# Performance work log

Measured on AMD Instinct MI355X. Metric: run time of the kernel, lower is better.

Reference implementation:

```python
import jax, jax.numpy as jnp
import numpy as np

B, T, H = 64, 512, 32
D_CONTENT, D_DISTORT, D_MOTION = 4096, 512, 256
D_TOTAL = D_CONTENT + D_DISTORT + D_MOTION  # 4864
RED = 128
TIME_INTERVAL = 8  # conf.ADJACENT_INTERVAL assumed
TAUS = (8, 10, 12, 14, 16)
BETA = 0.5


def setup_inputs() -> dict:
    key = jax.random.key(0)
    ks = jax.random.split(key, 20)
    s = 0.02
    f32 = jnp.float32
    return {
        "motionFeat": jax.random.normal(ks[0], (B, T, D_MOTION), f32),
        "featContent": jax.random.normal(ks[1], (B, T, D_CONTENT), f32),
        "featDistort": jax.random.normal(ks[2], (B, T, D_DISTORT), f32),
        "inputLength": jax.random.randint(ks[3], (B,), 200, T + 1),
        "fc0_w": jax.random.normal(ks[4], (RED, D_TOTAL), f32) * s,
        "fc0_b": jnp.zeros((RED,), f32),
        "gru_wih_f": jax.random.normal(ks[5], (3 * H, RED), f32) * s,
        "gru_whh_f": jax.random.normal(ks[6], (3 * H, H), f32) * s,
        "gru_bih_f": jnp.zeros((3 * H,), f32),
        "gru_bhh_f": jnp.zeros((3 * H,), f32),
        "gru_wih_b": jax.random.normal(ks[7], (3 * H, RED), f32) * s,
        "gru_whh_b": jax.random.normal(ks[8], (3 * H, H), f32) * s,
        "gru_bih_b": jnp.zeros((3 * H,), f32),
        "gru_bhh_b": jnp.zeros((3 * H,), f32),
        "q_w": jax.random.normal(ks[9], (1, 2 * H), f32) * s,
        "q_b": jnp.zeros((1,), f32),
        "mem1_w": jax.random.normal(ks[10], (32, 2 * H), f32) * s,
        "mem1_b": jnp.zeros((32,), f32),
        "mem2_w": jax.random.normal(ks[11], (5, 32), f32) * s,
        "mem2_b": jnp.zeros((5,), f32),
    }


def _gru_dir(xg, Whh, bhh, mask):
    """xg: [B,T,3H] precomputed input gates; mask: [B,T] bool. Returns [B,T,H]."""
    def step(h, inp):
        xgt, mt = inp  # [B,3H], [B]
        hg = h @ Whh.T + bhh
        r = jax.nn.sigmoid(xgt[:, :H] + hg[:, :H])
        z = jax.nn.sigmoid(xgt[:, H:2 * H] + hg[:, H:2 * H])
        n = jnp.tanh(xgt[:, 2 * H:] + r * hg[:, 2 * H:])
        hn = (1.0 - z) * n + z * h
        h = jnp.where(mt[:, None], hn, h)
        return h, h
    h0 = jnp.zeros((xg.shape[0], H), xg.dtype)
    _, out = jax.lax.scan(step, h0, (jnp.swapaxes(xg, 0, 1), jnp.swapaxes(mask, 0, 1)))
    return jnp.swapaxes(out, 0, 1)


def _tp_score(qv, maskf, vlen, tau, beta=BETA):
    """Vectorized TP() + mean over valid frames. qv,maskf: [B,T]; vlen: [B]."""
    Bq, Tq = qv.shape
    # l: causal running min over last tau frames (front pad +inf in q-space)
    qpad = jnp.concatenate([jnp.full((Bq, tau - 1), jnp.inf, qv.dtype), qv], axis=1)
    l = jnp.min(jnp.stack([qpad[:, k:k + Tq] for k in range(tau)], 0), axis=0)
    # m/n: forward exp-weighted average over next tau frames; padding qp=1e4 -> exp(-1e4)=0
    w = jnp.exp(-qv) * maskf
    num = qv * w
    zpad = jnp.zeros((Bq, tau - 1), qv.dtype)
    npad = jnp.concatenate([num, zpad], axis=1)
    wpad = jnp.concatenate([w, zpad], axis=1)
    msum = sum(npad[:, k:k + Tq] for k in range(tau))
    nsum = sum(wpad[:, k:k + Tq] for k in range(tau))
    ratio = jnp.where(nsum > 0, msum / jnp.where(nsum > 0, nsum, 1.0), 0.0)
    pooled = beta * ratio + (1.0 - beta) * l
    return jnp.sum(pooled * maskf, axis=1) / vlen.astype(qv.dtype)


def reference(motionFeat, featContent, featDistort, inputLength,
              fc0_w, fc0_b, gru_wih_f, gru_whh_f, gru_bih_f, gru_bhh_f,
              gru_wih_b, gru_whh_b, gru_bih_b, gru_bhh_b,
              q_w, q_b, mem1_w, mem1_b, mem2_w, mem2_b):
    total = jnp.concatenate([featContent, featDistort, motionFeat], axis=-1)  # [B,T,4864]
    scores = total @ fc0_w.T + fc0_b  # ANN with n_ANNlayers=1 -> just fc0
    vlen = inputLength - 2 * (TIME_INTERVAL // 2) - 1  # [B]
    t = jnp.arange(T)
    mask = t[None, :] < vlen[:, None]  # [B,T] bool
    maskf = mask.astype(scores.dtype)
    # forward GRU
    xg_f = scores @ gru_wih_f.T + gru_bih_f
    out_f = _gru_dir(xg_f, gru_whh_f, gru_bhh_f, mask)
    # backward GRU: reverse each sequence within its valid length
    rev = jnp.where(mask, vlen[:, None] - 1 - t[None, :], t[None, :])  # [B,T]
    x_rev = jnp.take_along_axis(scores, rev[:, :, None], axis=1)
    xg_b = x_rev @ gru_wih_b.T + gru_bih_b
    out_b_rev = _gru_dir(xg_b, gru_whh_b, gru_bhh_b, mask)
    out_b = jnp.take_along_axis(out_b_rev, rev[:, :, None], axis=1)
    outputs = jnp.concatenate([out_f, out_b], axis=-1) * maskf[:, :, None]  # [B,T,64]
    lastHidForward = jnp.take_along_axis(out_f, (vlen - 1)[:, None, None], axis=1)[:, 0]  # [B,32]
    lastHidBackward = out_b[:, 0]  # [B,32]
    q = (outputs @ q_w.T + q_b)[..., 0]  # [B,T]
    hidcat = jnp.concatenate([lastHidForward, lastHidBackward], axis=-1)
    h1 = jax.nn.relu(hidcat @ mem1_w.T + mem1_b)
    param = jax.nn.softmax(h1 @ mem2_w.T + mem2_b, axis=-1)  # [B,5]
    scores5 = jnp.stack([_tp_score(q, maskf, vlen, tau) for tau in TAUS], axis=-1)  # [B,5]
    one_hot = jax.nn.one_hot(jnp.argmax(param, axis=1), 5, dtype=scores5.dtype)
    finalScores = jnp.sum(one_hot * scores5, axis=-1)  # [B]
    return finalScores
```

## Files before the change

### kernel.cpp

```cpp
#include <hip/hip_runtime.h>

typedef float  floatx4  __attribute__((ext_vector_type(4)));
typedef float  floatx2  __attribute__((ext_vector_type(2)));
typedef __bf16 bf16x8   __attribute__((ext_vector_type(8)));
typedef unsigned short ushort8v __attribute__((ext_vector_type(8)));

constexpr int NB = 64;
constexpr int NT = 512;
constexpr int DC = 4096, DD = 512, DM = 256, DTOT = 4864;
constexpr int RED = 128;
constexpr int MROWS = NB * NT;

__device__ __forceinline__ unsigned short f2bf(float f) {
  unsigned u = __float_as_uint(f);
  unsigned r = u + 0x7FFFu + ((u >> 16) & 1u);
  return (unsigned short)(r >> 16);
}

__device__ __forceinline__ ushort8v pack8(floatx4 a, floatx4 b) {
  ushort8v u;
  u[0] = f2bf(a[0]); u[1] = f2bf(a[1]); u[2] = f2bf(a[2]); u[3] = f2bf(a[3]);
  u[4] = f2bf(b[0]); u[5] = f2bf(b[1]); u[6] = f2bf(b[2]); u[7] = f2bf(b[3]);
  return u;
}

template<int MODE>
__global__ __launch_bounds__(256, 2) void gemm_bt(
    const float* __restrict__ A0, const float* __restrict__ A1, const float* __restrict__ A2,
    const float* __restrict__ W0, const float* __restrict__ W1,
    const float* __restrict__ bias0, const float* __restrict__ bias1,
    float* __restrict__ outp)
{
  constexpr int BN   = (MODE == 0) ? 128 : 192;
  constexpr int KTOT = (MODE == 0) ? DTOT : RED;
  constexpr int WNT  = (MODE == 0) ? 2 : 3;
  constexpr int BK   = 128;
  constexpr int ACH  = 64 * (BK / 8) / 256;
  constexpr int WCH  = BN * (BK / 8) / 256;

  __shared__ __align__(16) unsigned short As[64 * BK];
  __shared__ __align__(16) unsigned short Ws[BN * BK];

  const int tid  = threadIdx.x;
  const int lane = tid & 63;
  const int wave = tid >> 6;
  const int m0   = blockIdx.x * 64;

  floatx4 pa[2 * ACH], pw[2 * WCH];

  auto loadA = [&](int k0) {
    #pragma unroll
    for (int c = 0; c < ACH; ++c) {
      const int g   = c * 256 + tid;
      const int row = g >> 4;
      const int kk  = (g & 15) * 8;
      const int m   = m0 + row;
      const float* src;
      if (MODE == 0) {
        const int k = k0 + kk;
        if (k < DC)           src = A0 + (size_t)m * DC + k;
        else if (k < DC + DD) src = A1 + (size_t)m * DD + (k - DC);
        else                  src = A2 + (size_t)m * DM + (k - DC - DD);
      } else {
        src = A0 + (size_t)m * RED + (k0 + kk);
      }
      pa[2 * c]     = *(const floatx4*)(src);
      pa[2 * c + 1] = *(const floatx4*)(src + 4);
    }
  };
  auto loadW = [&](int k0) {
    #pragma unroll
    for (int c = 0; c < WCH; ++c) {
      const int g   = c * 256 + tid;
      const int row = g >> 4;
      const int kk  = (g & 15) * 8;
      const float* src;
      if (MODE == 0) {
        src = W0 + (size_t)row * DTOT + (k0 + kk);
      } else {
        src = (row < 96) ? (W0 + (size_t)row * RED + (k0 + kk))
                         : (W1 + (size_t)(row - 96) * RED + (k0 + kk));
      }
      pw[2 * c]     = *(const floatx4*)(src);
      pw[2 * c + 1] = *(const floatx4*)(src + 4);
    }
  };
  auto storeA = [&]() {
    #pragma unroll
    for (int c = 0; c < ACH; ++c) {
      const int g   = c * 256 + tid;
      const int row = g >> 4;
      const int kk  = (g & 15) * 8;
      *(ushort8v*)&As[row * BK + (kk ^ ((row & 15) * 8))] = pack8(pa[2 * c], pa[2 * c + 1]);
    }
  };
  auto storeW = [&]() {
    #pragma unroll
    for (int c = 0; c < WCH; ++c) {
      const int g   = c * 256 + tid;
      const int row = g >> 4;
      const int kk  = (g & 15) * 8;
      *(ushort8v*)&Ws[row * BK + (kk ^ ((row & 15) * 8))] = pack8(pw[2 * c], pw[2 * c + 1]);
    }
  };

  floatx4 acc[4][WNT];
  #pragma unroll
  for (int mt = 0; mt < 4; ++mt)
    #pragma unroll
    for (int nt = 0; nt < WNT; ++nt)
      acc[mt][nt] = (floatx4){0.f, 0.f, 0.f, 0.f};

  const int lrow = lane & 15;
  const int lko  = (lane >> 4) * 8;

  loadA(0); loadW(0);

  for (int k0 = 0; k0 < KTOT; k0 += BK) {
    storeA(); storeW();
    __syncthreads();
    if (k0 + BK < KTOT) { loadA(k0 + BK); loadW(k0 + BK); }
    #pragma unroll
    for (int kk = 0; kk < BK; kk += 32) {
      bf16x8 af[4];
      #pragma unroll
      for (int mt = 0; mt < 4; ++mt) {
        const int row = mt * 16 + lrow;
        af[mt] = __builtin_bit_cast(bf16x8,
            *(const ushort8v*)&As[row * BK + ((kk + lko) ^ ((row & 15) * 8))]);
      }
      #pragma unroll
      for (int nt = 0; nt < WNT; ++nt) {
        const int wrow = (wave * WNT + nt) * 16 + lrow;
        bf16x8 wf = __builtin_bit_cast(bf16x8,
            *(const ushort8v*)&Ws[wrow * BK + ((kk + lko) ^ ((wrow & 15) * 8))]);
        #pragma unroll
        for (int mt = 0; mt < 4; ++mt)
          acc[mt][nt] = __builtin_amdgcn_mfma_f32_16x16x32_bf16(af[mt], wf, acc[mt][nt], 0, 0, 0);
      }
    }
    __syncthreads();
  }

  #pragma unroll
  for (int nt = 0; nt < WNT; ++nt) {
    const int n = (wave * WNT + nt) * 16 + lrow;
    const float bv = (MODE == 0) ? bias0[n]
                                 : ((n < 96) ? bias0[n] : bias1[n - 96]);
    #pragma unroll
    for (int mt = 0; mt < 4; ++mt) {
      const int mr = m0 + mt * 16 + (lane >> 4) * 4;
      #pragma unroll
      for (int r = 0; r < 4; ++r)
        outp[(size_t)(mr + r) * BN + n] = acc[mt][nt][r] + bv;
    }
  }
}

__global__ __launch_bounds__(64) void gru_kernel(
    const float* __restrict__ xg,
    const float* __restrict__ whh_f, const float* __restrict__ whh_b,
    const float* __restrict__ bhh_f, const float* __restrict__ bhh_b,
    const float* __restrict__ q_w,
    const int* __restrict__ inputLength,
    float* __restrict__ qpart,
    float* __restrict__ hid)
{
  const int b    = blockIdx.x >> 1;
  const int dir  = blockIdx.x & 1;
  const int l    = threadIdx.x;
  const int half = l >> 5;
  const int row  = l & 31;
  const int vlen = inputLength[b] - 9;

  const float* whh = dir ? whh_b : whh_f;
  const float* bhh = dir ? bhh_b : bhh_f;

  __shared__ __align__(16) float hsh[32];

  floatx2 wr[8], wz[8], wn[8];
  #pragma unroll
  for (int j = 0; j < 8; ++j) {
    const int c = 16 * half + 2 * j;
    wr[j] = *(const floatx2*)&whh[(size_t)row        * 32 + c];
    wz[j] = *(const floatx2*)&whh[(size_t)(32 + row) * 32 + c];
    wn[j] = *(const floatx2*)&whh[(size_t)(64 + row) * 32 + c];
  }
  const float br = bhh[row], bz = bhh[32 + row], bn = bhh[64 + row];
  const float qw = q_w[dir * 32 + row];

  if (l < 32) hsh[l] = 0.f;
  __syncthreads();

  auto xaddr = [&](int tt) {
    const int time = dir ? (vlen - 1 - tt) : tt;
    return xg + (size_t)(b * NT + time) * 192 + dir * 96;
  };
  float c_r = 0.f, c_z = 0.f, c_n = 0.f, n_r = 0.f, n_z = 0.f, n_n = 0.f;
  if (l < 32) {
    const float* x0 = xaddr(0);
    c_r = x0[l]; c_z = x0[32 + l]; c_n = x0[64 + l];
    if (vlen > 1) {
      const float* x1 = xaddr(1);
      n_r = x1[l]; n_z = x1[32 + l]; n_n = x1[64 + l];
    }
  }

  float* qout = qpart + (size_t)dir * (NB * NT) + (size_t)b * NT;

  float hl = 0.f;
  for (int t = 0; t < vlen; ++t) {
    const int time = dir ? (vlen - 1 - t) : t;

    float f_r = 0.f, f_z = 0.f, f_n = 0.f;
    if (t + 2 < vlen && l < 32) {
      const float* x2 = xaddr(t + 2);
      f_r = x2[l]; f_z = x2[32 + l]; f_n = x2[64 + l];
    }

    float h[16];
    #pragma unroll
    for (int i = 0; i < 4; ++i)
      *(floatx4*)&h[4 * i] = *(const floatx4*)&hsh[16 * half + 4 * i];
    const floatx2* h2 = (const floatx2*)h;

    floatx2 ar = {0.f, 0.f}, az = {0.f, 0.f}, an = {0.f, 0.f};
    floatx2 ar1 = {0.f, 0.f}, az1 = {0.f, 0.f}, an1 = {0.f, 0.f};
    #pragma unroll
    for (int j = 0; j < 4; ++j) {
      ar  += wr[j]     * h2[j];     ar1 += wr[4 + j] * h2[4 + j];
      az  += wz[j]     * h2[j];     az1 += wz[4 + j] * h2[4 + j];
      an  += wn[j]     * h2[j];     an1 += wn[4 + j] * h2[4 + j];
    }
    float pr = ar[0] + ar[1] + ar1[0] + ar1[1];
    float pz = az[0] + az[1] + az1[0] + az1[1];
    float pn = an[0] + an[1] + an1[0] + an1[1];
    pr += __shfl_xor(pr, 32);
    pz += __shfl_xor(pz, 32);
    pn += __shfl_xor(pn, 32);

    float hn = hl;
    if (l < 32) {
      const float r = 1.f / (1.f + __expf(-(c_r + pr + br)));
      const float z = 1.f / (1.f + __expf(-(c_z + pz + bz)));
      const float e = __expf(-2.f * (c_n + r * (pn + bn)));
      const float n = 2.f / (1.f + e) - 1.f;
      hn = (1.f - z) * n + z * hl;
      hl = hn;
      hsh[l] = hn;
    }

    float qp = (l < 32) ? hn * qw : 0.f;
    #pragma unroll
    for (int off = 16; off > 0; off >>= 1)
      qp += __shfl_xor(qp, off);
    if (l == 0) qout[time] = qp;

    if (t == vlen - 1 && l < 32) hid[b * 64 + dir * 32 + l] = hn;

    c_r = n_r; c_z = n_z; c_n = n_n;
    n_r = f_r; n_z = f_z; n_n = f_n;
  }
}

__global__ __launch_bounds__(64) void final_kernel(
    const float* __restrict__ qf, const float* __restrict__ qb,
    const float* __restrict__ hid,
    const float* __restrict__ q_b,
    const int* __restrict__ inputLength,
    const float* __restrict__ m1w, const float* __restrict__ m1b,
    const float* __restrict__ m2w, const float* __restrict__ m2b,
    float* __restrict__ fin)
{
  const int b = blockIdx.x;
  const int tid = threadIdx.x;
  const int vlen = inputLength[b] - 9;
  const float qb0 = q_b[0];

  __shared__ float qs[NT];
  __shared__ float es[NT];
  __shared__ float h1[32];
  __shared__ int tau_s;

  for (int t = tid; t < vlen; t += 64) {
    const float v = qf[b * NT + t] + qb[b * NT + t] + qb0;
    qs[t] = v;
    es[t] = expf(-v);
  }

  if (tid < 32) {
    const float* hf = hid + b * 64;
    const float* hb = hid + b * 64 + 32;
    float a = m1b[tid];
    #pragma unroll
    for (int j = 0; j < 32; ++j) a += m1w[tid * 64 + j] * hf[j];
    #pragma unroll
    for (int j = 0; j < 32; ++j) a += m1w[tid * 64 + 32 + j] * hb[j];
    h1[tid] = fmaxf(a, 0.f);
  }
  __syncthreads();
  if (tid == 0) {
    float best = -3.4e38f; int bi = 0;
    for (int i = 0; i < 5; ++i) {
      float lg = m2b[i];
      for (int j = 0; j < 32; ++j) lg += m2w[i * 32 + j] * h1[j];
      if (lg > best) { best = lg; bi = i; }
    }
    tau_s = 8 + 2 * bi;
  }
  __syncthreads();
  const int tau = tau_s;

  float partial = 0.f;
  for (int t = tid; t < vlen; t += 64) {
    float msum = 0.f, nsum = 0.f;
    const int kmax = (tau < vlen - t) ? tau : (vlen - t);
    for (int k = 0; k < kmax; ++k) { msum += qs[t + k] * es[t + k]; nsum += es[t + k]; }
    const float ratio = (nsum > 0.f) ? (msum / nsum) : 0.f;
    float l = 3.4e38f;
    const int kb = (tau <= t + 1) ? tau : (t + 1);
    for (int k = 0; k < kb; ++k) l = fminf(l, qs[t - k]);
    partial += 0.5f * ratio + 0.5f * l;
  }
  #pragma unroll
  for (int off = 32; off > 0; off >>= 1)
    partial += __shfl_down(partial, off);
  if (tid == 0) fin[b] = partial / (float)vlen;
}

extern "C" void kernel_launch(void* const* d_in, const int* in_sizes, int n_in,
                              void* d_out, int out_size, void* d_ws, size_t ws_size,
                              hipStream_t stream)
{
  const float* motion  = (const float*)d_in[0];
  const float* content = (const float*)d_in[1];
  const float* distort = (const float*)d_in[2];
  const int*   ilen    = (const int*)d_in[3];
  const float* fc0_w = (const float*)d_in[4];
  const float* fc0_b = (const float*)d_in[5];
  const float* wih_f = (const float*)d_in[6];
  const float* whh_f = (const float*)d_in[7];
  const float* bih_f = (const float*)d_in[8];
  const float* bhh_f = (const float*)d_in[9];
  const float* wih_b = (const float*)d_in[10];
  const float* whh_b = (const float*)d_in[11];
  const float* bih_b = (const float*)d_in[12];
  const float* bhh_b = (const float*)d_in[13];
  const float* q_w  = (const float*)d_in[14];
  const float* q_b  = (const float*)d_in[15];
  const float* m1w  = (const float*)d_in[16];
  const float* m1b  = (const float*)d_in[17];
  const float* m2w  = (const float*)d_in[18];
  const float* m2b  = (const float*)d_in[19];

  char* ws = (char*)d_ws;
  float* scores = (float*)(ws);
  float* xg     = (float*)(ws + (size_t)MROWS * RED * 4);
  float* qpart  = (float*)(ws + (size_t)MROWS * (RED + 192) * 4);
  float* hid    = (float*)(ws + (size_t)MROWS * (RED + 192) * 4
                              + (size_t)2 * MROWS * 4);

  gemm_bt<0><<<dim3(MROWS / 64), dim3(256), 0, stream>>>(
      content, distort, motion, fc0_w, nullptr, fc0_b, nullptr, scores);
  gemm_bt<1><<<dim3(MROWS / 64), dim3(256), 0, stream>>>(
      scores, nullptr, nullptr, wih_f, wih_b, bih_f, bih_b, xg);
  gru_kernel<<<dim3(NB * 2), dim3(64), 0, stream>>>(
      xg, whh_f, whh_b, bhh_f, bhh_b, q_w, ilen, qpart, hid);
  final_kernel<<<dim3(NB), dim3(64), 0, stream>>>(
      qpart, qpart + (size_t)NB * NT, hid, q_b, ilen, m1w, m1b, m2w, m2b, (float*)d_out);
}
```

Baseline: 1.116 ms.

## Fuse fc0 and GRU input-gate GEMMs; restructure GRU recurrence with LDS history

```diff
diff --git a/kernel.cpp b/kernel.cpp
--- a/kernel.cpp
+++ b/kernel.cpp
@@ -24,22 +24,19 @@
   return u;
 }
 
-template<int MODE>
-__global__ __launch_bounds__(256, 2) void gemm_bt(
+__global__ __launch_bounds__(256, 2) void gemm_fused(
     const float* __restrict__ A0, const float* __restrict__ A1, const float* __restrict__ A2,
-    const float* __restrict__ W0, const float* __restrict__ W1,
-    const float* __restrict__ bias0, const float* __restrict__ bias1,
-    float* __restrict__ outp)
+    const float* __restrict__ fc0w, const float* __restrict__ fc0b,
+    const float* __restrict__ wihf, const float* __restrict__ wihb,
+    const float* __restrict__ bihf, const float* __restrict__ bihb,
+    float* __restrict__ xg)
 {
-  constexpr int BN   = (MODE == 0) ? 128 : 192;
-  constexpr int KTOT = (MODE == 0) ? DTOT : RED;
-  constexpr int WNT  = (MODE == 0) ? 2 : 3;
-  constexpr int BK   = 128;
-  constexpr int ACH  = 64 * (BK / 8) / 256;
-  constexpr int WCH  = BN * (BK / 8) / 256;
+  constexpr int BK  = 128;
+  constexpr int ACH = 4;
+  constexpr int WCH = 8;
 
   __shared__ __align__(16) unsigned short As[64 * BK];
-  __shared__ __align__(16) unsigned short Ws[BN * BK];
+  __shared__ __align__(16) unsigned short Ws[192 * BK];
 
   const int tid  = threadIdx.x;
   const int lane = tid & 63;
@@ -55,15 +52,11 @@
       const int row = g >> 4;
       const int kk  = (g & 15) * 8;
       const int m   = m0 + row;
+      const int k   = k0 + kk;
       const float* src;
-      if (MODE == 0) {
-        const int k = k0 + kk;
-        if (k < DC)           src = A0 + (size_t)m * DC + k;
-        else if (k < DC + DD) src = A1 + (size_t)m * DD + (k - DC);
-        else                  src = A2 + (size_t)m * DM + (k - DC - DD);
-      } else {
-        src = A0 + (size_t)m * RED + (k0 + kk);
-      }
+      if (k < DC)           src = A0 + (size_t)m * DC + k;
+      else if (k < DC + DD) src = A1 + (size_t)m * DD + (k - DC);
+      else                  src = A2 + (size_t)m * DM + (k - DC - DD);
       pa[2 * c]     = *(const floatx4*)(src);
       pa[2 * c + 1] = *(const floatx4*)(src + 4);
     }
@@ -74,13 +67,7 @@
       const int g   = c * 256 + tid;
       const int row = g >> 4;
       const int kk  = (g & 15) * 8;
-      const float* src;
-      if (MODE == 0) {
-        src = W0 + (size_t)row * DTOT + (k0 + kk);
-      } else {
-        src = (row < 96) ? (W0 + (size_t)row * RED + (k0 + kk))
-                         : (W1 + (size_t)(row - 96) * RED + (k0 + kk));
-      }
+      const float* src = fc0w + (size_t)row * DTOT + (k0 + kk);
       pw[2 * c]     = *(const floatx4*)(src);
       pw[2 * c + 1] = *(const floatx4*)(src + 4);
     }
@@ -104,11 +91,11 @@
     }
   };
 
-  floatx4 acc[4][WNT];
+  floatx4 acc[4][2];
   #pragma unroll
   for (int mt = 0; mt < 4; ++mt)
     #pragma unroll
-    for (int nt = 0; nt < WNT; ++nt)
+    for (int nt = 0; nt < 2; ++nt)
       acc[mt][nt] = (floatx4){0.f, 0.f, 0.f, 0.f};
 
   const int lrow = lane & 15;
@@ -116,10 +103,10 @@
 
   loadA(0); loadW(0);
 
-  for (int k0 = 0; k0 < KTOT; k0 += BK) {
+  for (int k0 = 0; k0 < DTOT; k0 += BK) {
     storeA(); storeW();
     __syncthreads();
-    if (k0 + BK < KTOT) { loadA(k0 + BK); loadW(k0 + BK); }
+    if (k0 + BK < DTOT) { loadA(k0 + BK); loadW(k0 + BK); }
     #pragma unroll
     for (int kk = 0; kk < BK; kk += 32) {
       bf16x8 af[4];
@@ -130,8 +117,8 @@
             *(const ushort8v*)&As[row * BK + ((kk + lko) ^ ((row & 15) * 8))]);
       }
       #pragma unroll
-      for (int nt = 0; nt < WNT; ++nt) {
-        const int wrow = (wave * WNT + nt) * 16 + lrow;
+      for (int nt = 0; nt < 2; ++nt) {
+        const int wrow = (wave * 2 + nt) * 16 + lrow;
         bf16x8 wf = __builtin_bit_cast(bf16x8,
             *(const ushort8v*)&Ws[wrow * BK + ((kk + lko) ^ ((wrow & 15) * 8))]);
         #pragma unroll
@@ -143,16 +130,68 @@
   }
 
   #pragma unroll
-  for (int nt = 0; nt < WNT; ++nt) {
-    const int n = (wave * WNT + nt) * 16 + lrow;
-    const float bv = (MODE == 0) ? bias0[n]
-                                 : ((n < 96) ? bias0[n] : bias1[n - 96]);
+  for (int nt = 0; nt < 2; ++nt) {
+    const int n  = (wave * 2 + nt) * 16 + lrow;
+    const float bv = fc0b[n];
+    #pragma unroll
+    for (int mt = 0; mt < 4; ++mt) {
+      const int rb = mt * 16 + (lane >> 4) * 4;
+      #pragma unroll
+      for (int r = 0; r < 4; ++r) {
+        const int row = rb + r;
+        As[row * BK + (n ^ ((row & 15) * 8))] = f2bf(acc[mt][nt][r] + bv);
+      }
+    }
+  }
+  #pragma unroll
+  for (int c = 0; c < 12; ++c) {
+    const int g   = c * 256 + tid;
+    const int row = g >> 4;
+    const int kk  = (g & 15) * 8;
+    const float* src = (row < 96) ? (wihf + (size_t)row * RED + kk)
+                                  : (wihb + (size_t)(row - 96) * RED + kk);
+    floatx4 u0 = *(const floatx4*)src, u1 = *(const floatx4*)(src + 4);
+    *(ushort8v*)&Ws[row * BK + (kk ^ ((row & 15) * 8))] = pack8(u0, u1);
+  }
+  __syncthreads();
+
+  floatx4 acc2[4][3];
+  #pragma unroll
+  for (int mt = 0; mt < 4; ++mt)
+    #pragma unroll
+    for (int nt = 0; nt < 3; ++nt)
+      acc2[mt][nt] = (floatx4){0.f, 0.f, 0.f, 0.f};
+
+  #pragma unroll
+  for (int kk = 0; kk < BK; kk += 32) {
+    bf16x8 af[4];
+    #pragma unroll
+    for (int mt = 0; mt < 4; ++mt) {
+      const int row = mt * 16 + lrow;
+      af[mt] = __builtin_bit_cast(bf16x8,
+          *(const ushort8v*)&As[row * BK + ((kk + lko) ^ ((row & 15) * 8))]);
+    }
+    #pragma unroll
+    for (int nt = 0; nt < 3; ++nt) {
+      const int wrow = (wave * 3 + nt) * 16 + lrow;
+      bf16x8 wf = __builtin_bit_cast(bf16x8,
+          *(const ushort8v*)&Ws[wrow * BK + ((kk + lko) ^ ((wrow & 15) * 8))]);
+      #pragma unroll
+      for (int mt = 0; mt < 4; ++mt)
+        acc2[mt][nt] = __builtin_amdgcn_mfma_f32_16x16x32_bf16(af[mt], wf, acc2[mt][nt], 0, 0, 0);
+    }
+  }
+
+  #pragma unroll
+  for (int nt = 0; nt < 3; ++nt) {
+    const int n  = (wave * 3 + nt) * 16 + lrow;
+    const float bv = (n < 96) ? bihf[n] : bihb[n - 96];
     #pragma unroll
     for (int mt = 0; mt < 4; ++mt) {
       const int mr = m0 + mt * 16 + (lane >> 4) * 4;
       #pragma unroll
       for (int r = 0; r < 4; ++r)
-        outp[(size_t)(mr + r) * BN + n] = acc[mt][nt][r] + bv;
+        xg[(size_t)(mr + r) * 192 + n] = acc2[mt][nt][r] + bv;
     }
   }
 }
@@ -166,31 +205,34 @@
     float* __restrict__ qpart,
     float* __restrict__ hid)
 {
+  constexpr int HP = 36;
   const int b    = blockIdx.x >> 1;
   const int dir  = blockIdx.x & 1;
   const int l    = threadIdx.x;
-  const int half = l >> 5;
   const int row  = l & 31;
   const int vlen = inputLength[b] - 9;
 
   const float* whh = dir ? whh_b : whh_f;
   const float* bhh = dir ? bhh_b : bhh_f;
 
-  __shared__ __align__(16) float hsh[32];
-
-  floatx2 wr[8], wz[8], wn[8];
-  #pragma unroll
-  for (int j = 0; j < 8; ++j) {
-    const int c = 16 * half + 2 * j;
-    wr[j] = *(const floatx2*)&whh[(size_t)row        * 32 + c];
-    wz[j] = *(const floatx2*)&whh[(size_t)(32 + row) * 32 + c];
-    wn[j] = *(const floatx2*)&whh[(size_t)(64 + row) * 32 + c];
-  }
-  const float br = bhh[row], bz = bhh[32 + row], bn = bhh[64 + row];
-  const float qw = q_w[dir * 32 + row];
-
-  if (l < 32) hsh[l] = 0.f;
-  __syncthreads();
+  __shared__ __align__(16) float hbuf[NT * HP];
+
+  floatx2 wr[16], wz[16], wn[16];
+  float br = 0.f, bz = 0.f, bn = 0.f;
+  if (l < 32) {
+    #pragma unroll
+    for (int j = 0; j < 16; ++j) {
+      wr[j] = *(const floatx2*)&whh[(size_t)row        * 32 + 2 * j];
+      wz[j] = *(const floatx2*)&whh[(size_t)(32 + row) * 32 + 2 * j];
+      wn[j] = *(const floatx2*)&whh[(size_t)(64 + row) * 32 + 2 * j];
+    }
+    br = bhh[row]; bz = bhh[32 + row]; bn = bhh[64 + row];
+  } else {
+    #pragma unroll
+    for (int j = 0; j < 16; ++j) {
+      wr[j] = (floatx2){0.f, 0.f}; wz[j] = (floatx2){0.f, 0.f}; wn[j] = (floatx2){0.f, 0.f};
+    }
+  }
 
   auto xaddr = [&](int tt) {
     const int time = dir ? (vlen - 1 - tt) : tt;
@@ -200,13 +242,9 @@
   if (l < 32) {
     const float* x0 = xaddr(0);
     c_r = x0[l]; c_z = x0[32 + l]; c_n = x0[64 + l];
-    if (vlen > 1) {
-      const float* x1 = xaddr(1);
-      n_r = x1[l]; n_z = x1[32 + l]; n_n = x1[64 + l];
-    }
-  }
-
-  float* qout = qpart + (size_t)dir * (NB * NT) + (size_t)b * NT;
+    const float* x1 = xaddr(1);
+    n_r = x1[l]; n_z = x1[32 + l]; n_n = x1[64 + l];
+  }
 
   float hl = 0.f;
   for (int t = 0; t < vlen; ++t) {
@@ -218,48 +256,57 @@
       f_r = x2[l]; f_z = x2[32 + l]; f_n = x2[64 + l];
     }
 
-    float h[16];
-    #pragma unroll
-    for (int i = 0; i < 4; ++i)
-      *(floatx4*)&h[4 * i] = *(const floatx4*)&hsh[16 * half + 4 * i];
+    float h[32];
+    if (t == 0) {
+      #pragma unroll
+      for (int j = 0; j < 32; ++j) h[j] = 0.f;
+    } else {
+      const int pt = dir ? (time + 1) : (time - 1);
+      const float* hp = &hbuf[pt * HP];
+      #pragma unroll
+      for (int i = 0; i < 8; ++i)
+        *(floatx4*)&h[4 * i] = *(const floatx4*)&hp[4 * i];
+    }
     const floatx2* h2 = (const floatx2*)h;
 
-    floatx2 ar = {0.f, 0.f}, az = {0.f, 0.f}, an = {0.f, 0.f};
+    floatx2 ar0 = {0.f, 0.f}, az0 = {0.f, 0.f}, an0 = {0.f, 0.f};
     floatx2 ar1 = {0.f, 0.f}, az1 = {0.f, 0.f}, an1 = {0.f, 0.f};
     #pragma unroll
-    for (int j = 0; j < 4; ++j) {
-      ar  += wr[j]     * h2[j];     ar1 += wr[4 + j] * h2[4 + j];
-      az  += wz[j]     * h2[j];     az1 += wz[4 + j] * h2[4 + j];
-      an  += wn[j]     * h2[j];     an1 += wn[4 + j] * h2[4 + j];
-    }
-    float pr = ar[0] + ar[1] + ar1[0] + ar1[1];
-    float pz = az[0] + az[1] + az1[0] + az1[1];
-    float pn = an[0] + an[1] + an1[0] + an1[1];
-    pr += __shfl_xor(pr, 32);
-    pz += __shfl_xor(pz, 32);
-    pn += __shfl_xor(pn, 32);
-
-    float hn = hl;
+    for (int j = 0; j < 8; ++j) {
+      ar0 += wr[j] * h2[j];     ar1 += wr[8 + j] * h2[8 + j];
+      az0 += wz[j] * h2[j];     az1 += wz[8 + j] * h2[8 + j];
+      an0 += wn[j] * h2[j];     an1 += wn[8 + j] * h2[8 + j];
+    }
+    const float pr = ar0[0] + ar0[1] + ar1[0] + ar1[1];
+    const float pz = az0[0] + az0[1] + az1[0] + az1[1];
+    const float pn = an0[0] + an0[1] + an1[0] + an1[1];
+
     if (l < 32) {
       const float r = 1.f / (1.f + __expf(-(c_r + pr + br)));
       const float z = 1.f / (1.f + __expf(-(c_z + pz + bz)));
       const float e = __expf(-2.f * (c_n + r * (pn + bn)));
       const float n = 2.f / (1.f + e) - 1.f;
-      hn = (1.f - z) * n + z * hl;
+      const float hn = (1.f - z) * n + z * hl;
       hl = hn;
-      hsh[l] = hn;
-    }
-
-    float qp = (l < 32) ? hn * qw : 0.f;
-    #pragma unroll
-    for (int off = 16; off > 0; off >>= 1)
-      qp += __shfl_xor(qp, off);
-    if (l == 0) qout[time] = qp;
-
-    if (t == vlen - 1 && l < 32) hid[b * 64 + dir * 32 + l] = hn;
+      hbuf[time * HP + l] = hn;
+      if (t == vlen - 1) hid[b * 64 + dir * 32 + l] = hn;
+    }
 
     c_r = n_r; c_z = n_z; c_n = n_n;
     n_r = f_r; n_z = f_z; n_n = f_n;
+  }
+
+  float qwv[32];
+  #pragma unroll
+  for (int i = 0; i < 8; ++i)
+    *(floatx4*)&qwv[4 * i] = *(const floatx4*)&q_w[dir * 32 + 4 * i];
+  float* qout = qpart + (size_t)dir * (NB * NT) + (size_t)b * NT;
+  for (int t = l; t < vlen; t += 64) {
+    const float* hr = &hbuf[t * HP];
+    float a0 = 0.f, a1 = 0.f;
+    #pragma unroll
+    for (int j = 0; j < 16; ++j) { a0 += hr[j] * qwv[j]; a1 += hr[16 + j] * qwv[16 + j]; }
+    qout[t] = a0 + a1;
   }
 }
 
@@ -354,16 +401,12 @@
   const float* m2b  = (const float*)d_in[19];
 
   char* ws = (char*)d_ws;
-  float* scores = (float*)(ws);
-  float* xg     = (float*)(ws + (size_t)MROWS * RED * 4);
-  float* qpart  = (float*)(ws + (size_t)MROWS * (RED + 192) * 4);
-  float* hid    = (float*)(ws + (size_t)MROWS * (RED + 192) * 4
-                              + (size_t)2 * MROWS * 4);
-
-  gemm_bt<0><<<dim3(MROWS / 64), dim3(256), 0, stream>>>(
-      content, distort, motion, fc0_w, nullptr, fc0_b, nullptr, scores);
-  gemm_bt<1><<<dim3(MROWS / 64), dim3(256), 0, stream>>>(
-      scores, nullptr, nullptr, wih_f, wih_b, bih_f, bih_b, xg);
+  float* xg    = (float*)(ws);
+  float* qpart = (float*)(ws + (size_t)MROWS * 192 * 4);
+  float* hid   = (float*)(ws + (size_t)MROWS * 192 * 4 + (size_t)2 * MROWS * 4);
+
+  gemm_fused<<<dim3(MROWS / 64), dim3(256), 0, stream>>>(
+      content, distort, motion, fc0_w, fc0_b, wih_f, wih_b, bih_f, bih_b, xg);
   gru_kernel<<<dim3(NB * 2), dim3(64), 0, stream>>>(
       xg, whh_f, whh_b, bhh_f, bhh_b, q_w, ilen, qpart, hid);
   final_kernel<<<dim3(NB), dim3(64), 0, stream>>>(
```

Measured after the change: 1.075 ms. 1.04x faster.
